# Optimization experiments

Hardware: AMD Instinct MI355X
Metric: run time of the kernel (lower is better)

## Reference

```python
import jax, jax.numpy as jnp
import numpy as np

D_MODEL = 256
NHEAD = 8
D_K = D_MODEL // NHEAD
IM_SIZE = 8
SCALE = float(IM_SIZE ** 2)  # sqrt(im_size**4)


def setup_inputs() -> dict:
    key = jax.random.key(0)
    ks = jax.random.split(key, 9)
    B, P, S = 8, 256, 8
    s = 1.0 / np.sqrt(D_MODEL)
    return {
        "x": jax.random.normal(ks[0], (B, P, S, S, D_MODEL), jnp.float32),
        "Wq": jax.random.normal(ks[1], (D_MODEL, D_MODEL), jnp.float32) * s,
        "bq": jax.random.normal(ks[2], (D_MODEL,), jnp.float32) * s,
        "Wk": jax.random.normal(ks[3], (D_MODEL, D_MODEL), jnp.float32) * s,
        "bk": jax.random.normal(ks[4], (D_MODEL,), jnp.float32) * s,
        "Wv": jax.random.normal(ks[5], (D_MODEL, D_MODEL), jnp.float32) * s,
        "bv": jax.random.normal(ks[6], (D_MODEL,), jnp.float32) * s,
        "Wo": jax.random.normal(ks[7], (D_MODEL, D_MODEL), jnp.float32) * s,
        "bo": jax.random.normal(ks[8], (D_MODEL,), jnp.float32) * s,
    }


def _split_heads(t):
    # torch: view(..., d_k, nhead).permute(0,5,1,2,3,4) -> [b, n, p, x, y, d_k]
    b, p, sx, sy, _ = t.shape
    t = t.reshape(b, p, sx, sy, D_K, NHEAD)
    return jnp.transpose(t, (0, 5, 1, 2, 3, 4))


def reference(x, Wq, bq, Wk, bk, Wv, bv, Wo, bo):
    Q = _split_heads(x @ Wq.T + bq)
    K = _split_heads(x @ Wk.T + bk)
    V = _split_heads(x @ Wv.T + bv)
    # scores over flattened (x, y, d_k) dims
    scores = jnp.einsum('bnpxyd,bnqxyd->bnpq', Q, K) / SCALE
    attn = jax.nn.softmax(scores, axis=-1)
    out = jnp.einsum('bnpq,bnqxyd->bnpxyd', attn, V)
    # permute to [b, p, x, y, d_k, n] then merge (d_k, n) -> d_model
    out = jnp.transpose(out, (0, 2, 3, 4, 5, 1))
    b, p, sx, sy, _, _ = out.shape
    out = out.reshape(b, p, sx, sy, NHEAD * D_K)
    return out @ Wo.T + bo
```

## Files before the change

### kernel.cpp

```cpp
#include <hip/hip_runtime.h>
#include <hip/hip_bf16.h>


typedef __bf16 bf16;
typedef __attribute__((ext_vector_type(8))) __bf16 bf16x8;
typedef __attribute__((ext_vector_type(4))) float floatx4;
typedef __attribute__((ext_vector_type(8))) unsigned short ushort8;

#define CDIM 2048

static __device__ __forceinline__ floatx4 mfma16(bf16x8 a, bf16x8 b, floatx4 c) {
  return __builtin_amdgcn_mfma_f32_16x16x32_bf16(a, b, c, 0, 0, 0);
}

static __device__ __forceinline__ void gload_lds16(const void* g, void* l) {
  __builtin_amdgcn_global_load_lds((const __attribute__((address_space(1))) void*)g,
                                   (__attribute__((address_space(3))) void*)l, 16, 0, 0);
}

__global__ __launch_bounds__(256) void k0_prep(
    const float* __restrict__ Wq, const float* __restrict__ bq,
    const float* __restrict__ Wk, const float* __restrict__ bk,
    const float* __restrict__ Wv, const float* __restrict__ bv,
    const float* __restrict__ Wo,
    bf16* __restrict__ Wp, bf16* __restrict__ Wk3, float* __restrict__ biasp)
{
  const int bid = blockIdx.x, tid = threadIdx.x;
  int g = (bid & 31) * 256 + tid;
  int lane = g & 63, rowblk = (g >> 6) & 15, kk = g >> 10;
  int h = lane >> 4, cl = lane & 15;
  int d0 = kk * 32 + 8 * h;
  if (bid < 32) {
    int ip = rowblk * 16 + cl;
    int isrc = ((ip & 31) << 3) | (ip >> 5);
#pragma unroll
    for (int mat = 0; mat < 3; mat++) {
      const float* W = (mat == 0) ? Wq : (mat == 1) ? Wk : Wv;
      bf16x8 v;
#pragma unroll
      for (int j = 0; j < 8; j++) v[j] = (bf16)W[isrc * 256 + d0 + j];
      *reinterpret_cast<bf16x8*>(Wp + ((size_t)mat * 8192 + g) * 8) = v;
    }
    if (bid == 0 && tid < 256) {
      int bs = ((tid & 31) << 3) | (tid >> 5);
      biasp[tid] = bq[bs]; biasp[256 + tid] = bk[bs]; biasp[512 + tid] = bv[bs];
    }
  } else {
    int j = rowblk * 16 + cl;
    bf16x8 v;
#pragma unroll
    for (int jj = 0; jj < 8; jj++) {
      int c = d0 + jj;
      v[jj] = (bf16)Wo[j * 256 + (((c & 31) << 3) | (c >> 5))];
    }
    *reinterpret_cast<bf16x8*>(Wk3 + (size_t)g * 8) = v;
  }
}

__global__ __launch_bounds__(512, 4) void k1_qkv(
    const float* __restrict__ x, const bf16* __restrict__ Wp,
    const float* __restrict__ biasp,
    bf16* __restrict__ Qs, bf16* __restrict__ Ks, bf16* __restrict__ Vt)
{
  __shared__ bf16 buf[2][64 * 256];
  const int bx = blockIdx.x;
  const int tid = threadIdx.x;
  const int lane = tid & 63;
  const int w = tid >> 6;
  const int h = lane >> 4, cl = lane & 15;
  const int c7 = cl & 7;

  floatx4 sreg[8];

#define K1_LOAD(VB)                                                          \
  {                                                                          \
    int a_ = (VB) / 24;                                                      \
    int t0_ = (a_ * 8 + ((VB) & 7)) * 64;                                    \
    _Pragma("unroll")                                                        \
    for (int k = 0; k < 4; ++k) {                                            \
      int G = k * 512 + tid;                                                 \
      int row = G >> 5;                                                      \
      const float* sp = x + (size_t)(t0_ + row) * 256 + (G & 31) * 8;        \
      sreg[2 * k]     = *reinterpret_cast<const floatx4*>(sp);               \
      sreg[2 * k + 1] = *reinterpret_cast<const floatx4*>(sp + 4);           \
    }                                                                        \
  }

#define K1_CVTWRITE(BUFI)                                                    \
  {                                                                          \
    _Pragma("unroll")                                                        \
    for (int k = 0; k < 4; ++k) {                                            \
      int G = k * 512 + tid;                                                 \
      int row = G >> 5;                                                      \
      bf16x8 v;                                                              \
      _Pragma("unroll")                                                      \
      for (int j = 0; j < 4; j++) {                                          \
        v[j] = (bf16)sreg[2 * k][j];                                         \
        v[4 + j] = (bf16)sreg[2 * k + 1][j];                                 \
      }                                                                      \
      int Gp = (G & ~7) | ((G ^ row) & 7);                                   \
      *reinterpret_cast<bf16x8*>(&buf[BUFI][Gp * 8]) = v;                    \
    }                                                                        \
  }

#define K1_COMPUTE(VB, BUFI)                                                 \
  {                                                                          \
    int a_ = (VB) / 24;                                                      \
    int rem_ = (VB) - a_ * 24;                                               \
    int mat_ = rem_ >> 3;                                                    \
    int t0_ = (a_ * 8 + (rem_ & 7)) * 64;                                    \
    const bf16* Wm = Wp + (size_t)mat_ * 65536;                              \
    floatx4 acc[4][2];                                                       \
    _Pragma("unroll")                                                        \
    for (int i = 0; i < 4; i++)                                              \
      _Pragma("unroll")                                                      \
      for (int j = 0; j < 2; j++) acc[i][j] = (floatx4)0.0f;                 \
    _Pragma("unroll 2")                                                      \
    for (int kk = 0; kk < 8; ++kk) {                                         \
      bf16x8 av[4];                                                          \
      _Pragma("unroll")                                                      \
      for (int mt = 0; mt < 4; mt++) {                                       \
        int rr = mt * 16 + cl;                                               \
        int G = rr * 32 + kk * 4 + h;                                        \
        int Gp = (G & ~7) | ((G ^ c7) & 7);                                  \
        av[mt] = *reinterpret_cast<const bf16x8*>(&buf[BUFI][Gp * 8]);       \
      }                                                                      \
      bf16x8 b0 = *reinterpret_cast<const bf16x8*>(                          \
          Wm + ((size_t)(kk * 16 + w * 2 + 0) * 64 + lane) * 8);             \
      bf16x8 b1 = *reinterpret_cast<const bf16x8*>(                          \
          Wm + ((size_t)(kk * 16 + w * 2 + 1) * 64 + lane) * 8);             \
      _Pragma("unroll")                                                      \
      for (int mt = 0; mt < 4; mt++) acc[mt][0] = mfma16(av[mt], b0, acc[mt][0]); \
      _Pragma("unroll")                                                      \
      for (int mt = 0; mt < 4; mt++) acc[mt][1] = mfma16(av[mt], b1, acc[mt][1]); \
    }                                                                        \
    int b_ = t0_ >> 14;                                                      \
    int p_ = (t0_ >> 6) & 255;                                               \
    if (mat_ < 2) {                                                          \
      bf16* ob = ((mat_ == 0) ? Qs : Ks) + ((size_t)(b_ * 8 + w) * 256 + p_) * 2048; \
      _Pragma("unroll")                                                      \
      for (int nt = 0; nt < 2; nt++) {                                       \
        const int ip = w * 32 + nt * 16 + cl;                                \
        const float bb = biasp[mat_ * 256 + ip];                             \
        const int dk = nt * 16 + cl;                                         \
        _Pragma("unroll")                                                    \
        for (int mt = 0; mt < 4; mt++)                                       \
          _Pragma("unroll")                                                  \
          for (int r = 0; r < 4; r++) {                                      \
            int sxy = mt * 16 + 4 * h + r;                                   \
            ob[sxy * 32 + dk] = (bf16)(acc[mt][nt][r] + bb);                 \
          }                                                                  \
      }                                                                      \
    } else {                                                                 \
      _Pragma("unroll")                                                      \
      for (int nt = 0; nt < 2; nt++) {                                       \
        const int ip = w * 32 + nt * 16 + cl;                                \
        const float bb = biasp[512 + ip];                                    \
        _Pragma("unroll")                                                    \
        for (int mt = 0; mt < 4; mt++)                                       \
          _Pragma("unroll")                                                  \
          for (int r = 0; r < 4; r++) {                                      \
            int t = t0_ + mt * 16 + 4 * h + r;                               \
            Vt[(size_t)t * 256 + ip] = (bf16)(acc[mt][nt][r] + bb);          \
          }                                                                  \
      }                                                                      \
    }                                                                        \
  }

  K1_LOAD(bx);
  K1_CVTWRITE(0);
  __syncthreads();
#pragma unroll
  for (int u = 1; u < 4; ++u) {
    K1_LOAD(bx + u * 1536);
    K1_COMPUTE(bx + (u - 1) * 1536, (u - 1) & 1);
    __syncthreads();
    K1_CVTWRITE(u & 1);
    __syncthreads();
  }
  K1_COMPUTE(bx + 3 * 1536, 1);

#undef K1_LOAD
#undef K1_CVTWRITE
#undef K1_COMPUTE
}

__global__ __launch_bounds__(1024, 1) void k2a_scores(
    const bf16* __restrict__ Qs, const bf16* __restrict__ Ks,
    bf16* __restrict__ attn)
{
  __shared__ bf16 Qch[2][64 * 64];
  __shared__ bf16 Kch[2][256 * 64];
  __shared__ float redmax[4][4][16];
  __shared__ float redsum[4][4][16];

  const int bx = blockIdx.x;
  const int bn = bx & 63;
  const int p0 = (bx >> 6) * 64;
  const int tid = threadIdx.x;
  const int lane = tid & 63;
  const int w = tid >> 6;
  const int wr = w >> 2, wc = w & 3;
  const int h = lane >> 4, cl = lane & 15;

  const bf16* Qb = Qs + (size_t)bn * 524288 + (size_t)p0 * 2048;
  const bf16* Kb = Ks + (size_t)bn * 524288;

  const int rq = tid >> 3, sq = (tid & 7) ^ (rq & 7);
  const size_t qsrc = (size_t)rq * 2048 + sq * 8;
  int rk[2]; size_t ksrc[2];
#pragma unroll
  for (int i = 0; i < 2; ++i) {
    int L = i * 1024 + tid;
    rk[i] = L >> 3;
    int s = (L & 7) ^ (rk[i] & 7);
    ksrc[i] = (size_t)rk[i] * 2048 + s * 8;
  }

#define K2A_STAGE(bufi, c)                                                  \
  {                                                                         \
    if (tid < 512) gload_lds16(Qb + qsrc + (c) * 64, &Qch[bufi][(w * 64) * 8]); \
    gload_lds16(Kb + ksrc[0] + (c) * 64, &Kch[bufi][(w * 64) * 8]);         \
    gload_lds16(Kb + ksrc[1] + (c) * 64, &Kch[bufi][(1024 + w * 64) * 8]);  \
  }

  floatx4 acc[4];
#pragma unroll
  for (int j = 0; j < 4; j++) acc[j] = (floatx4)0.0f;

  K2A_STAGE(0, 0);
  __syncthreads();
  int buf = 0;
  for (int c = 0; c < 32; ++c) {
    if (c + 1 < 32) K2A_STAGE(buf ^ 1, c + 1);
#pragma unroll
    for (int kk = 0; kk < 2; ++kk) {
      bf16x8 av, bv[4];
      {
        int row = wr * 16 + cl;
        int gg = kk * 4 + h;
        av = *reinterpret_cast<const bf16x8*>(
            &Qch[buf][(row * 8 + (gg ^ (row & 7))) * 8]);
      }
#pragma unroll
      for (int nt = 0; nt < 4; nt++) {
        int row = wc * 64 + nt * 16 + cl;
        int gg = kk * 4 + h;
        bv[nt] = *reinterpret_cast<const bf16x8*>(
            &Kch[buf][(row * 8 + (gg ^ (row & 7))) * 8]);
      }
#pragma unroll
      for (int nt = 0; nt < 4; nt++) acc[nt] = mfma16(av, bv[nt], acc[nt]);
    }
    __syncthreads();
    buf ^= 1;
  }

  float pm[4];
#pragma unroll
  for (int r = 0; r < 4; r++)
    pm[r] = fmaxf(fmaxf(acc[0][r], acc[1][r]), fmaxf(acc[2][r], acc[3][r]));
#pragma unroll
  for (int off = 1; off < 16; off <<= 1)
#pragma unroll
    for (int r = 0; r < 4; r++)
      pm[r] = fmaxf(pm[r], __shfl_xor(pm[r], off, 64));
  if (cl == 0) {
#pragma unroll
    for (int r = 0; r < 4; r++) redmax[wr][wc][4 * h + r] = pm[r];
  }
  __syncthreads();

  float gm[4], ps[4];
#pragma unroll
  for (int r = 0; r < 4; r++) {
    int row = 4 * h + r;
    gm[r] = fmaxf(fmaxf(redmax[wr][0][row], redmax[wr][1][row]),
                  fmaxf(redmax[wr][2][row], redmax[wr][3][row]));
    ps[r] = 0.0f;
  }
  const float KS = 1.44269504088896340736f / 64.0f;
#pragma unroll
  for (int nt = 0; nt < 4; nt++)
#pragma unroll
    for (int r = 0; r < 4; r++) {
      float e = exp2f((acc[nt][r] - gm[r]) * KS);
      acc[nt][r] = e;
      ps[r] += e;
    }
#pragma unroll
  for (int off = 1; off < 16; off <<= 1)
#pragma unroll
    for (int r = 0; r < 4; r++) ps[r] += __shfl_xor(ps[r], off, 64);
  if (cl == 0) {
#pragma unroll
    for (int r = 0; r < 4; r++) redsum[wr][wc][4 * h + r] = ps[r];
  }
  __syncthreads();

#pragma unroll
  for (int r = 0; r < 4; r++) {
    int row = 4 * h + r;
    float gs = (redsum[wr][0][row] + redsum[wr][1][row])
             + (redsum[wr][2][row] + redsum[wr][3][row]);
    ps[r] = 1.0f / gs;
  }
#pragma unroll
  for (int nt = 0; nt < 4; nt++) {
    int q = wc * 64 + nt * 16 + cl;
#pragma unroll
    for (int r = 0; r < 4; r++) {
      int row = p0 + wr * 16 + 4 * h + r;
      attn[(size_t)bn * 65536 + row * 256 + q] = (bf16)(acc[nt][r] * ps[r]);
    }
  }
#undef K2A_STAGE
}

__global__ __launch_bounds__(256) void k2t_transpose(
    const bf16* __restrict__ Vtok, bf16* __restrict__ Vq)
{
  const int bx = blockIdx.x;
  const int bn = bx & 63;
  const int r2 = bx >> 6;
  const int q0 = (r2 & 3) * 64;
  const int c0 = (r2 >> 2) * 64;
  const int b = bn >> 3, n = bn & 7;
  __shared__ unsigned short tile[64][65];
  const unsigned short* src = (const unsigned short*)Vtok;
  unsigned short* dst = (unsigned short*)Vq + (size_t)bn * 524288;
  {
    const int q = threadIdx.x >> 3;
    const int cj = (threadIdx.x & 7) * 8;
    const int c = c0 + cj;
    const int sxy = c >> 5, dk0 = c & 31;
#pragma unroll
    for (int it = 0; it < 2; ++it) {
      int qq = q + it * 32;
      size_t sa = (size_t)((b * 256 + q0 + qq) * 64 + sxy) * 256 + n * 32 + dk0;
      ushort8 s = *reinterpret_cast<const ushort8*>(src + sa);
#pragma unroll
      for (int j = 0; j < 8; j++) tile[qq][cj + j] = s[j];
    }
  }
  __syncthreads();
  {
    const int crow = threadIdx.x >> 2;
    const int qj = (threadIdx.x & 3) * 8;
#pragma unroll
    for (int it = 0; it < 2; ++it) {
      int qq = qj + it * 32;
      ushort8 sv;
#pragma unroll
      for (int j = 0; j < 8; j++) sv[j] = tile[qq + j][crow];
      *reinterpret_cast<ushort8*>(dst + (size_t)(c0 + crow) * 256 + q0 + qq) = sv;
    }
  }
}

__global__ __launch_bounds__(512, 6) void k2b_pv(
    const bf16* __restrict__ attn, const bf16* __restrict__ Vq,
    bf16* __restrict__ yhat)
{
  __shared__ bf16 As[64 * 256];
  const int bx = blockIdx.x;
  const int bn = bx & 63;
  const int r2 = bx >> 6;
  const int p0 = (r2 & 3) * 64;
  const int c0 = (r2 >> 2) * 256;
  const int b = bn >> 3, n = bn & 7;
  const int tid = threadIdx.x;
  const int lane = tid & 63;
  const int w = tid >> 6;
  const int h = lane >> 4, cl = lane & 15;
  const int c7 = cl & 7;

  const bf16* Ab = attn + (size_t)bn * 65536 + (size_t)p0 * 256;
  const bf16* Vb = Vq + (size_t)bn * 524288;

#pragma unroll
  for (int i = 0; i < 4; ++i) {
    int L = (i * 8 + w) * 64 + lane;
    int S = (L & ~7) | ((L ^ (L >> 5)) & 7);
    gload_lds16(Ab + (size_t)S * 8, &As[(size_t)(i * 8 + w) * 64 * 8]);
  }
  __syncthreads();

  floatx4 acc[4][2];
#pragma unroll
  for (int i = 0; i < 4; i++)
#pragma unroll
    for (int j = 0; j < 2; j++) acc[i][j] = (floatx4)0.0f;

#pragma unroll 2
  for (int kk = 0; kk < 8; ++kk) {
    bf16x8 av[4];
#pragma unroll
    for (int mt = 0; mt < 4; mt++) {
      int rr = mt * 16 + cl;
      int G = rr * 32 + kk * 4 + h;
      int Gp = (G & ~7) | ((G ^ c7) & 7);
      av[mt] = *reinterpret_cast<const bf16x8*>(&As[Gp * 8]);
    }
    bf16x8 b0 = *reinterpret_cast<const bf16x8*>(
        Vb + (size_t)(c0 + w * 32 + cl) * 256 + kk * 32 + 8 * h);
    bf16x8 b1 = *reinterpret_cast<const bf16x8*>(
        Vb + (size_t)(c0 + w * 32 + 16 + cl) * 256 + kk * 32 + 8 * h);
#pragma unroll
    for (int mt = 0; mt < 4; mt++) acc[mt][0] = mfma16(av[mt], b0, acc[mt][0]);
#pragma unroll
    for (int mt = 0; mt < 4; mt++) acc[mt][1] = mfma16(av[mt], b1, acc[mt][1]);
  }

#pragma unroll
  for (int nt = 0; nt < 2; nt++) {
    const int cg = c0 + w * 32 + nt * 16 + cl;
    const int dk = cg & 31, sxy = cg >> 5;
#pragma unroll
    for (int mt = 0; mt < 4; mt++)
#pragma unroll
      for (int r = 0; r < 4; r++) {
        int p = p0 + mt * 16 + 4 * h + r;
        size_t t = (size_t)((b * 256 + p) * 64) + sxy;
        yhat[t * 256 + n * 32 + dk] = (bf16)acc[mt][nt][r];
      }
  }
}

__global__ __launch_bounds__(512, 6) void k3_out(
    const bf16* __restrict__ yhat, const bf16* __restrict__ Wk3,
    const float* __restrict__ bo, float* __restrict__ outp)
{
  __shared__ bf16 As[64 * 256];
  const int t0 = blockIdx.x * 64;
  const int tid = threadIdx.x;
  const int lane = tid & 63;
  const int w = tid >> 6;
  const int h = lane >> 4, cl = lane & 15;
  const int c7 = cl & 7;

  const bf16* Ab = yhat + (size_t)t0 * 256;

#pragma unroll
  for (int i = 0; i < 4; ++i) {
    int L = (i * 8 + w) * 64 + lane;
    int S = (L & ~7) | ((L ^ (L >> 5)) & 7);
    gload_lds16(Ab + (size_t)S * 8, &As[(size_t)(i * 8 + w) * 64 * 8]);
  }
  __syncthreads();

  floatx4 acc[4][2];
#pragma unroll
  for (int i = 0; i < 4; i++)
#pragma unroll
    for (int j = 0; j < 2; j++) acc[i][j] = (floatx4)0.0f;

#pragma unroll 2
  for (int kk = 0; kk < 8; ++kk) {
    bf16x8 av[4];
#pragma unroll
    for (int mt = 0; mt < 4; mt++) {
      int rr = mt * 16 + cl;
      int G = rr * 32 + kk * 4 + h;
      int Gp = (G & ~7) | ((G ^ c7) & 7);
      av[mt] = *reinterpret_cast<const bf16x8*>(&As[Gp * 8]);
    }
    bf16x8 b0 = *reinterpret_cast<const bf16x8*>(
        Wk3 + ((size_t)(kk * 16 + w * 2 + 0) * 64 + lane) * 8);
    bf16x8 b1 = *reinterpret_cast<const bf16x8*>(
        Wk3 + ((size_t)(kk * 16 + w * 2 + 1) * 64 + lane) * 8);
#pragma unroll
    for (int mt = 0; mt < 4; mt++) acc[mt][0] = mfma16(av[mt], b0, acc[mt][0]);
#pragma unroll
    for (int mt = 0; mt < 4; mt++) acc[mt][1] = mfma16(av[mt], b1, acc[mt][1]);
  }

#pragma unroll
  for (int nt = 0; nt < 2; nt++) {
    const int j = w * 32 + nt * 16 + cl;
    const float bb = bo[j];
#pragma unroll
    for (int mt = 0; mt < 4; mt++)
#pragma unroll
      for (int r = 0; r < 4; r++)
        outp[(size_t)(t0 + mt * 16 + 4 * h + r) * 256 + j] = acc[mt][nt][r] + bb;
  }
}

extern "C" void kernel_launch(void* const* d_in, const int* in_sizes, int n_in,
                              void* d_out, int out_size, void* d_ws, size_t ws_size,
                              hipStream_t stream) {
  const float* x  = (const float*)d_in[0];
  const float* Wq = (const float*)d_in[1];
  const float* bq = (const float*)d_in[2];
  const float* Wk = (const float*)d_in[3];
  const float* bk = (const float*)d_in[4];
  const float* Wv = (const float*)d_in[5];
  const float* bv = (const float*)d_in[6];
  const float* Wo = (const float*)d_in[7];
  const float* bo = (const float*)d_in[8];
  float* outp = (float*)d_out;

  char* ws = (char*)d_ws;
  const size_t SZ_QKV = 67108864;
  size_t off = 0;
  bf16* Qs   = (bf16*)(ws + off); off += SZ_QKV;
  bf16* Ks   = (bf16*)(ws + off); off += SZ_QKV;
  bf16* Vtok = (bf16*)(ws + off); off += SZ_QKV;
  bf16* attn = (bf16*)(ws + off); off += 8388608;
  bf16* Wp   = (bf16*)(ws + off); off += 393216;
  bf16* Wk3  = (bf16*)(ws + off); off += 131072;
  float* biasp = (float*)(ws + off); off += 3072;
  if (ws_size < off) return;

  bf16* yhat = Qs;
  bf16* Vq   = Ks;

  k0_prep<<<64, 256, 0, stream>>>(Wq, bq, Wk, bk, Wv, bv, Wo, Wp, Wk3, biasp);
  k1_qkv<<<1536, 512, 0, stream>>>(x, Wp, biasp, Qs, Ks, Vtok);
  k2a_scores<<<256, 1024, 0, stream>>>(Qs, Ks, attn);
  k2t_transpose<<<8192, 256, 0, stream>>>(Vtok, Vq);
  k2b_pv<<<2048, 512, 0, stream>>>(attn, Vq, yhat);
  k3_out<<<2048, 512, 0, stream>>>(yhat, Wk3, bo, outp);
}
```

Measured before the change: 298.2 us.

## Fuse V transpose into QKV projection epilogue via LDS staging

The separate V transpose kernel is removed. The QKV kernel now splits its blocks into Q/K blocks and V blocks. V blocks load tiles grouped by spatial position across 64 patches, stage the projected output in LDS with an XOR swizzle, and write it directly in the [b,n,c,q] layout that the PV kernel consumes. This avoids a full write and re-read of the 64MB token-major V buffer and one kernel launch. In exchange the V path does strided x loads (one 1KB row per patch) and adds extra LDS passes and barriers.

```diff
diff --git a/kernel.cpp b/kernel.cpp
--- a/kernel.cpp
+++ b/kernel.cpp
@@ -60,7 +60,7 @@
 __global__ __launch_bounds__(512, 4) void k1_qkv(
     const float* __restrict__ x, const bf16* __restrict__ Wp,
     const float* __restrict__ biasp,
-    bf16* __restrict__ Qs, bf16* __restrict__ Ks, bf16* __restrict__ Vt)
+    bf16* __restrict__ Qs, bf16* __restrict__ Ks, bf16* __restrict__ Vq)
 {
   __shared__ bf16 buf[2][64 * 256];
   const int bx = blockIdx.x;
@@ -71,11 +71,46 @@
   const int c7 = cl & 7;
 
   floatx4 sreg[8];
-
-#define K1_LOAD(VB)                                                          \
-  {                                                                          \
-    int a_ = (VB) / 24;                                                      \
-    int t0_ = (a_ * 8 + ((VB) & 7)) * 64;                                    \
+  floatx4 acc[4][2];
+
+#define K1_CVTWRITE(BUFI)                                                    \
+  {                                                                          \
+    _Pragma("unroll")                                                        \
+    for (int k = 0; k < 4; ++k) {                                            \
+      int G = k * 512 + tid;                                                 \
+      int row = G >> 5;                                                      \
+      bf16x8 v;                                                              \
+      _Pragma("unroll")                                                      \
+      for (int j = 0; j < 4; j++) {                                          \
+        v[j] = (bf16)sreg[2 * k][j];                                         \
+        v[4 + j] = (bf16)sreg[2 * k + 1][j];                                 \
+      }                                                                      \
+      int Gp = (G & ~7) | ((G ^ row) & 7);                                   \
+      *reinterpret_cast<bf16x8*>(&buf[BUFI][Gp * 8]) = v;                    \
+    }                                                                        \
+  }
+
+#define K1_AFRAG(BUFI, KK, AV)                                               \
+  {                                                                          \
+    _Pragma("unroll")                                                        \
+    for (int mt = 0; mt < 4; mt++) {                                         \
+      int rr = mt * 16 + cl;                                                 \
+      int G = rr * 32 + (KK) * 4 + h;                                        \
+      int Gp = (G & ~7) | ((G ^ c7) & 7);                                    \
+      AV[mt] = *reinterpret_cast<const bf16x8*>(&buf[BUFI][Gp * 8]);         \
+    }                                                                        \
+  }
+
+  if (bx < 1024) {
+#define KQK_DEC(VB)                                                          \
+    int a_ = (VB) >> 4;                                                      \
+    int mat_ = ((VB) >> 3) & 1;                                              \
+    int t0_ = (a_ * 8 + ((VB) & 7)) * 64;
+
+#define KQK_LOAD(VB)                                                         \
+  {                                                                          \
+    KQK_DEC(VB)                                                              \
+    (void)mat_;                                                              \
     _Pragma("unroll")                                                        \
     for (int k = 0; k < 4; ++k) {                                            \
       int G = k * 512 + tid;                                                 \
@@ -86,31 +121,10 @@
     }                                                                        \
   }
 
-#define K1_CVTWRITE(BUFI)                                                    \
-  {                                                                          \
-    _Pragma("unroll")                                                        \
-    for (int k = 0; k < 4; ++k) {                                            \
-      int G = k * 512 + tid;                                                 \
-      int row = G >> 5;                                                      \
-      bf16x8 v;                                                              \
-      _Pragma("unroll")                                                      \
-      for (int j = 0; j < 4; j++) {                                          \
-        v[j] = (bf16)sreg[2 * k][j];                                         \
-        v[4 + j] = (bf16)sreg[2 * k + 1][j];                                 \
-      }                                                                      \
-      int Gp = (G & ~7) | ((G ^ row) & 7);                                   \
-      *reinterpret_cast<bf16x8*>(&buf[BUFI][Gp * 8]) = v;                    \
-    }                                                                        \
-  }
-
-#define K1_COMPUTE(VB, BUFI)                                                 \
-  {                                                                          \
-    int a_ = (VB) / 24;                                                      \
-    int rem_ = (VB) - a_ * 24;                                               \
-    int mat_ = rem_ >> 3;                                                    \
-    int t0_ = (a_ * 8 + (rem_ & 7)) * 64;                                    \
+#define KQK_COMPUTE(VB, BUFI)                                                \
+  {                                                                          \
+    KQK_DEC(VB)                                                              \
     const bf16* Wm = Wp + (size_t)mat_ * 65536;                              \
-    floatx4 acc[4][2];                                                       \
     _Pragma("unroll")                                                        \
     for (int i = 0; i < 4; i++)                                              \
       _Pragma("unroll")                                                      \
@@ -118,13 +132,7 @@
     _Pragma("unroll 2")                                                      \
     for (int kk = 0; kk < 8; ++kk) {                                         \
       bf16x8 av[4];                                                          \
-      _Pragma("unroll")                                                      \
-      for (int mt = 0; mt < 4; mt++) {                                       \
-        int rr = mt * 16 + cl;                                               \
-        int G = rr * 32 + kk * 4 + h;                                        \
-        int Gp = (G & ~7) | ((G ^ c7) & 7);                                  \
-        av[mt] = *reinterpret_cast<const bf16x8*>(&buf[BUFI][Gp * 8]);       \
-      }                                                                      \
+      K1_AFRAG(BUFI, kk, av)                                                 \
       bf16x8 b0 = *reinterpret_cast<const bf16x8*>(                          \
           Wm + ((size_t)(kk * 16 + w * 2 + 0) * 64 + lane) * 8);             \
       bf16x8 b1 = *reinterpret_cast<const bf16x8*>(                          \
@@ -136,53 +144,139 @@
     }                                                                        \
     int b_ = t0_ >> 14;                                                      \
     int p_ = (t0_ >> 6) & 255;                                               \
-    if (mat_ < 2) {                                                          \
-      bf16* ob = ((mat_ == 0) ? Qs : Ks) + ((size_t)(b_ * 8 + w) * 256 + p_) * 2048; \
-      _Pragma("unroll")                                                      \
-      for (int nt = 0; nt < 2; nt++) {                                       \
-        const int ip = w * 32 + nt * 16 + cl;                                \
-        const float bb = biasp[mat_ * 256 + ip];                             \
-        const int dk = nt * 16 + cl;                                         \
+    bf16* ob = ((mat_ == 0) ? Qs : Ks) + ((size_t)(b_ * 8 + w) * 256 + p_) * 2048; \
+    _Pragma("unroll")                                                        \
+    for (int nt = 0; nt < 2; nt++) {                                         \
+      const int ip = w * 32 + nt * 16 + cl;                                  \
+      const float bb = biasp[mat_ * 256 + ip];                               \
+      const int dk = nt * 16 + cl;                                           \
+      _Pragma("unroll")                                                      \
+      for (int mt = 0; mt < 4; mt++)                                         \
         _Pragma("unroll")                                                    \
-        for (int mt = 0; mt < 4; mt++)                                       \
-          _Pragma("unroll")                                                  \
-          for (int r = 0; r < 4; r++) {                                      \
-            int sxy = mt * 16 + 4 * h + r;                                   \
-            ob[sxy * 32 + dk] = (bf16)(acc[mt][nt][r] + bb);                 \
-          }                                                                  \
-      }                                                                      \
-    } else {                                                                 \
-      _Pragma("unroll")                                                      \
-      for (int nt = 0; nt < 2; nt++) {                                       \
-        const int ip = w * 32 + nt * 16 + cl;                                \
-        const float bb = biasp[512 + ip];                                    \
+        for (int r = 0; r < 4; r++) {                                        \
+          int sxy = mt * 16 + 4 * h + r;                                     \
+          ob[sxy * 32 + dk] = (bf16)(acc[mt][nt][r] + bb);                   \
+        }                                                                    \
+    }                                                                        \
+  }
+
+    KQK_LOAD(bx);
+    K1_CVTWRITE(0);
+    __syncthreads();
+#pragma unroll
+    for (int u = 1; u < 4; ++u) {
+      KQK_LOAD(bx + u * 1024);
+      KQK_COMPUTE(bx + (u - 1) * 1024, (u - 1) & 1);
+      __syncthreads();
+      K1_CVTWRITE(u & 1);
+      __syncthreads();
+    }
+    KQK_COMPUTE(bx + 3 * 1024, 1);
+#undef KQK_DEC
+#undef KQK_LOAD
+#undef KQK_COMPUTE
+  } else {
+    const int bxv = bx - 1024;
+#define KV_DEC(VB)                                                           \
+    int b_ = (VB) >> 8;                                                      \
+    int sxy_ = ((VB) >> 2) & 63;                                             \
+    int pblk_ = (VB) & 3;
+
+#define KV_LOAD(VB)                                                          \
+  {                                                                          \
+    KV_DEC(VB)                                                               \
+    _Pragma("unroll")                                                        \
+    for (int k = 0; k < 4; ++k) {                                            \
+      int G = k * 512 + tid;                                                 \
+      int row = G >> 5;                                                      \
+      const float* sp = x +                                                  \
+          (size_t)((b_ * 256 + pblk_ * 64 + row) * 64 + sxy_) * 256 + (G & 31) * 8; \
+      sreg[2 * k]     = *reinterpret_cast<const floatx4*>(sp);               \
+      sreg[2 * k + 1] = *reinterpret_cast<const floatx4*>(sp + 4);           \
+    }                                                                        \
+  }
+
+#define KV_COMPUTE(BUFI)                                                     \
+  {                                                                          \
+    const bf16* Wm = Wp + (size_t)2 * 65536;                                 \
+    _Pragma("unroll")                                                        \
+    for (int i = 0; i < 4; i++)                                              \
+      _Pragma("unroll")                                                      \
+      for (int j = 0; j < 2; j++) acc[i][j] = (floatx4)0.0f;                 \
+    _Pragma("unroll 2")                                                      \
+    for (int kk = 0; kk < 8; ++kk) {                                         \
+      bf16x8 av[4];                                                          \
+      K1_AFRAG(BUFI, kk, av)                                                 \
+      bf16x8 b0 = *reinterpret_cast<const bf16x8*>(                          \
+          Wm + ((size_t)(kk * 16 + w * 2 + 0) * 64 + lane) * 8);             \
+      bf16x8 b1 = *reinterpret_cast<const bf16x8*>(                          \
+          Wm + ((size_t)(kk * 16 + w * 2 + 1) * 64 + lane) * 8);             \
+      _Pragma("unroll")                                                      \
+      for (int mt = 0; mt < 4; mt++) acc[mt][0] = mfma16(av[mt], b0, acc[mt][0]); \
+      _Pragma("unroll")                                                      \
+      for (int mt = 0; mt < 4; mt++) acc[mt][1] = mfma16(av[mt], b1, acc[mt][1]); \
+    }                                                                        \
+  }
+
+#define KV_EPI_LDS(BUFI)                                                     \
+  {                                                                          \
+    _Pragma("unroll")                                                        \
+    for (int nt = 0; nt < 2; nt++) {                                         \
+      const int ip = w * 32 + nt * 16 + cl;                                  \
+      const float bb = biasp[512 + ip];                                      \
+      const int sx = 8 * (ip & 7);                                           \
+      _Pragma("unroll")                                                      \
+      for (int mt = 0; mt < 4; mt++)                                         \
         _Pragma("unroll")                                                    \
-        for (int mt = 0; mt < 4; mt++)                                       \
-          _Pragma("unroll")                                                  \
-          for (int r = 0; r < 4; r++) {                                      \
-            int t = t0_ + mt * 16 + 4 * h + r;                               \
-            Vt[(size_t)t * 256 + ip] = (bf16)(acc[mt][nt][r] + bb);          \
-          }                                                                  \
-      }                                                                      \
-    }                                                                        \
-  }
-
-  K1_LOAD(bx);
-  K1_CVTWRITE(0);
-  __syncthreads();
-#pragma unroll
-  for (int u = 1; u < 4; ++u) {
-    K1_LOAD(bx + u * 1536);
-    K1_COMPUTE(bx + (u - 1) * 1536, (u - 1) & 1);
+        for (int r = 0; r < 4; r++) {                                        \
+          int pl = mt * 16 + 4 * h + r;                                      \
+          buf[BUFI][ip * 64 + (pl ^ sx)] = (bf16)(acc[mt][nt][r] + bb);      \
+        }                                                                    \
+    }                                                                        \
+  }
+
+#define KV_EPI_STORE(VB, BUFI)                                               \
+  {                                                                          \
+    KV_DEC(VB)                                                               \
+    _Pragma("unroll")                                                        \
+    for (int j = 0; j < 4; ++j) {                                            \
+      int ip_ = j * 64 + (tid >> 3);                                         \
+      int c8 = tid & 7;                                                      \
+      int pb = c8 ^ (ip_ & 7);                                               \
+      ushort8 v = *reinterpret_cast<const ushort8*>(                         \
+          &buf[BUFI][ip_ * 64 + pb * 8]);                                    \
+      int n_ = ip_ >> 5, dk_ = ip_ & 31;                                     \
+      *reinterpret_cast<ushort8*>(Vq + (size_t)(b_ * 8 + n_) * 524288        \
+          + (size_t)(sxy_ * 32 + dk_) * 256 + pblk_ * 64 + c8 * 8) = v;      \
+    }                                                                        \
+  }
+
+    KV_LOAD(bxv);
+    K1_CVTWRITE(0);
     __syncthreads();
-    K1_CVTWRITE(u & 1);
+#pragma unroll
+    for (int u = 1; u < 4; ++u) {
+      KV_LOAD(bxv + u * 512);
+      KV_COMPUTE((u - 1) & 1);
+      __syncthreads();
+      KV_EPI_LDS((u - 1) & 1);
+      K1_CVTWRITE(u & 1);
+      __syncthreads();
+      KV_EPI_STORE(bxv + (u - 1) * 512, (u - 1) & 1);
+    }
+    KV_COMPUTE(1);
     __syncthreads();
-  }
-  K1_COMPUTE(bx + 3 * 1536, 1);
-
-#undef K1_LOAD
+    KV_EPI_LDS(1);
+    __syncthreads();
+    KV_EPI_STORE(bxv + 3 * 512, 1);
+#undef KV_DEC
+#undef KV_LOAD
+#undef KV_COMPUTE
+#undef KV_EPI_LDS
+#undef KV_EPI_STORE
+  }
 #undef K1_CVTWRITE
-#undef K1_COMPUTE
+#undef K1_AFRAG
 }
 
 __global__ __launch_bounds__(1024, 1) void k2a_scores(
@@ -315,47 +409,6 @@
     }
   }
 #undef K2A_STAGE
-}
-
-__global__ __launch_bounds__(256) void k2t_transpose(
-    const bf16* __restrict__ Vtok, bf16* __restrict__ Vq)
-{
-  const int bx = blockIdx.x;
-  const int bn = bx & 63;
-  const int r2 = bx >> 6;
-  const int q0 = (r2 & 3) * 64;
-  const int c0 = (r2 >> 2) * 64;
-  const int b = bn >> 3, n = bn & 7;
-  __shared__ unsigned short tile[64][65];
-  const unsigned short* src = (const unsigned short*)Vtok;
-  unsigned short* dst = (unsigned short*)Vq + (size_t)bn * 524288;
-  {
-    const int q = threadIdx.x >> 3;
-    const int cj = (threadIdx.x & 7) * 8;
-    const int c = c0 + cj;
-    const int sxy = c >> 5, dk0 = c & 31;
-#pragma unroll
-    for (int it = 0; it < 2; ++it) {
-      int qq = q + it * 32;
-      size_t sa = (size_t)((b * 256 + q0 + qq) * 64 + sxy) * 256 + n * 32 + dk0;
-      ushort8 s = *reinterpret_cast<const ushort8*>(src + sa);
-#pragma unroll
-      for (int j = 0; j < 8; j++) tile[qq][cj + j] = s[j];
-    }
-  }
-  __syncthreads();
-  {
-    const int crow = threadIdx.x >> 2;
-    const int qj = (threadIdx.x & 3) * 8;
-#pragma unroll
-    for (int it = 0; it < 2; ++it) {
-      int qq = qj + it * 32;
-      ushort8 sv;
-#pragma unroll
-      for (int j = 0; j < 8; j++) sv[j] = tile[qq + j][crow];
-      *reinterpret_cast<ushort8*>(dst + (size_t)(c0 + crow) * 256 + q0 + qq) = sv;
-    }
-  }
 }
 
 __global__ __launch_bounds__(512, 6) void k2b_pv(
@@ -506,7 +559,7 @@
   size_t off = 0;
   bf16* Qs   = (bf16*)(ws + off); off += SZ_QKV;
   bf16* Ks   = (bf16*)(ws + off); off += SZ_QKV;
-  bf16* Vtok = (bf16*)(ws + off); off += SZ_QKV;
+  bf16* Vq   = (bf16*)(ws + off); off += SZ_QKV;
   bf16* attn = (bf16*)(ws + off); off += 8388608;
   bf16* Wp   = (bf16*)(ws + off); off += 393216;
   bf16* Wk3  = (bf16*)(ws + off); off += 131072;
@@ -514,12 +567,10 @@
   if (ws_size < off) return;
 
   bf16* yhat = Qs;
-  bf16* Vq   = Ks;
 
   k0_prep<<<64, 256, 0, stream>>>(Wq, bq, Wk, bk, Wv, bv, Wo, Wp, Wk3, biasp);
-  k1_qkv<<<1536, 512, 0, stream>>>(x, Wp, biasp, Qs, Ks, Vtok);
+  k1_qkv<<<1536, 512, 0, stream>>>(x, Wp, biasp, Qs, Ks, Vq);
   k2a_scores<<<256, 1024, 0, stream>>>(Qs, Ks, attn);
-  k2t_transpose<<<8192, 256, 0, stream>>>(Vtok, Vq);
   k2b_pv<<<2048, 512, 0, stream>>>(attn, Vq, yhat);
   k3_out<<<2048, 512, 0, stream>>>(yhat, Wk3, bo, outp);
 }
```

Result: slower. 325.4 us (+9.1%).
